# Performance work log

Measured on AMD Instinct MI355X. Metric: run time of the kernel, lower is better.

Reference implementation:

```python
import jax, jax.numpy as jnp
import numpy as np

B, S, D, H = 2, 2048, 768, 12
HD = D // H  # head dim = 64

def setup_inputs() -> dict:
    key = jax.random.key(0)
    ks = jax.random.split(key, 9)
    s = 1.0 / np.sqrt(D)
    return {
        "x": jax.random.normal(ks[0], (B, S, D), dtype=jnp.float32),
        "Wq": jax.random.uniform(ks[1], (D, D), jnp.float32, -s, s),
        "bq": jax.random.uniform(ks[2], (D,), jnp.float32, -s, s),
        "Wk": jax.random.uniform(ks[3], (D, D), jnp.float32, -s, s),
        "bk": jax.random.uniform(ks[4], (D,), jnp.float32, -s, s),
        "Wv": jax.random.uniform(ks[5], (D, D), jnp.float32, -s, s),
        "bv": jax.random.uniform(ks[6], (D,), jnp.float32, -s, s),
        "Wo": jax.random.uniform(ks[7], (D, D), jnp.float32, -s, s),
        "bo": jax.random.uniform(ks[8], (D,), jnp.float32, -s, s),
    }

def reference(x, Wq, bq, Wk, bk, Wv, bv, Wo, bo):
    b, s, _ = x.shape
    # linear projections, split into heads: [b, h, s, hd]
    def proj(W, bias):
        y = x @ W + bias
        return y.reshape(b, s, H, HD).transpose(0, 2, 1, 3)
    q = proj(Wq, bq)
    k = proj(Wk, bk)
    v = proj(Wv, bv)
    scale = 1.0 / np.sqrt(HD).astype(np.float32)
    scores = jnp.einsum('bhqd,bhkd->bhqk', q, k) * scale
    attn = jax.nn.softmax(scores, axis=-1)
    out = jnp.einsum('bhqk,bhkd->bhqd', attn, v)
    out = out.transpose(0, 2, 1, 3).reshape(b, s, D)
    return out @ Wo + bo
```

## Files before the change

kernel.cpp:

```cpp
#include <hip/hip_runtime.h>
#include <math.h>

#define NH 12
#define SEQ 2048
#define DM 768
#define HD 64
#define NB 2
#define MT (NB * SEQ)
#define QSCL 0.18033688011112042591999058512524f

typedef short bf16x8 __attribute__((ext_vector_type(8)));
typedef float f32x16 __attribute__((ext_vector_type(16)));
typedef unsigned u32x2 __attribute__((ext_vector_type(2)));

__device__ __forceinline__ unsigned short bf16_rne(float x) {
    unsigned u = __float_as_uint(x);
    u += 0x7fffu + ((u >> 16) & 1u);
    return (unsigned short)(u >> 16);
}
__device__ __forceinline__ float bf16_tof(short h) {
    return __uint_as_float(((unsigned)(unsigned short)h) << 16);
}
__device__ __forceinline__ unsigned cvtpk(float lo, float hi) {
    unsigned r;
    asm("v_cvt_pk_bf16_f32 %0, %1, %2" : "=v"(r) : "v"(lo), "v"(hi));
    return r;
}

__device__ __forceinline__ void gl_lds16(const void* g, void* s) {
    __builtin_amdgcn_global_load_lds(
        (const __attribute__((address_space(1))) unsigned int*)g,
        (__attribute__((address_space(3))) unsigned int*)s, 16, 0, 0);
}

__device__ __forceinline__ f32x16 mfma32(bf16x8 a, bf16x8 b, f32x16 c) {
    return __builtin_amdgcn_mfma_f32_32x32x16_bf16(a, b, c, 0, 0, 0);
}

__device__ __forceinline__ bf16x8 gfrag(const char* base, int row, int physblk) {
    return *(const bf16x8*)(base + row * 64 + physblk * 16);
}
__device__ __forceinline__ bf16x8 afrag(const short* base, int row, int blk) {
    return *(const bf16x8*)(base + row * 64 + ((blk ^ (row & 7)) << 3));
}

__global__ __launch_bounds__(256)
void conv_all(const float* __restrict__ x,
              const float* __restrict__ Wq, const float* __restrict__ Wk,
              const float* __restrict__ Wv, const float* __restrict__ Wo,
              short* __restrict__ xg, short* __restrict__ wqkv,
              short* __restrict__ wo)
{
    int b = blockIdx.x;
    if (b < 1536) {
        const int idx = b * 256 + threadIdx.x;
        const int m = idx / 96, bk = idx % 96;
        const float* src = x + (size_t)m * DM + bk * 8;
        float4 v0 = *(const float4*)src;
        float4 v1 = *(const float4*)(src + 4);
        const float vv[8] = {v0.x, v0.y, v0.z, v0.w, v1.x, v1.y, v1.z, v1.w};
        union { short s[8]; int4 q; } hh;
#pragma unroll
        for (int j = 0; j < 8; j++) hh.s[j] = (short)bf16_rne(vv[j]);
        const int pb = (bk & ~3) | ((bk & 3) ^ ((m >> 1) & 3));
        *(int4*)(xg + (size_t)m * DM + pb * 8) = hh.q;
    } else {
        b -= 1536;
        const int z = b / 288;
        const float* __restrict__ W = (z == 0) ? Wq : (z == 1) ? Wk : (z == 2) ? Wv : Wo;
        short* __restrict__ wdst = (z == 3) ? wo : (wqkv + (size_t)z * 589824);
        const int idx = (b % 288) * 256 + threadIdx.x;
        const int n = idx % 768, bk = idx / 768;
        union { short s[8]; int4 q; } hh;
#pragma unroll
        for (int j = 0; j < 8; j++) hh.s[j] = (short)bf16_rne(W[(size_t)(bk * 8 + j) * DM + n]);
        const int pb = (bk & ~3) | ((bk & 3) ^ ((n >> 1) & 3));
        *(int4*)(wdst + (size_t)n * DM + pb * 8) = hh.q;
    }
}

template<bool SWAP>
__device__ __forceinline__ void qkv_loop(const char* pA, const char* pB,
                                         char* As, char* Bs,
                                         int t, f32x16* acc)
{
    const int w = t >> 6, l = t & 63;
    const int q32 = l & 31, half = l >> 5;
    const int sel = (q32 >> 1) & 3;
    const int arow  = 32 * (w & 1) + q32;
    const int brow0 = 64 * (w >> 1) + q32;
    char* dA = As + t * 16;
    char* dB = Bs + t * 16;

    uint4 a0, b00, b10;
    uint4 a1, b01, b11;

    a0  = *(const uint4*)(pA);
    b00 = *(const uint4*)(pB);
    b10 = *(const uint4*)(pB + 64 * 1536);
    a1  = *(const uint4*)(pA + 64);
    b01 = *(const uint4*)(pB + 64);
    b11 = *(const uint4*)(pB + 64 * 1536 + 64);
    *(uint4*)dA = a0;
    *(uint4*)dB = b00;
    *(uint4*)(dB + 4096) = b10;
    __syncthreads();

    auto compute = [&](const char* sA, const char* sB) {
#pragma unroll
        for (int s = 0; s < 2; s++) {
            const int blk = (s * 2 + half) ^ sel;
            bf16x8 a  = gfrag(sA, arow, blk);
            bf16x8 b0 = gfrag(sB, brow0, blk);
            bf16x8 b1 = gfrag(sB, brow0 + 32, blk);
            if (SWAP) {
                acc[0] = mfma32(b0, a, acc[0]);
                acc[1] = mfma32(b1, a, acc[1]);
            } else {
                acc[0] = mfma32(a, b0, acc[0]);
                acc[1] = mfma32(a, b1, acc[1]);
            }
        }
    };

    for (int kb = 0; kb < 12; kb++) {
        if (kb < 11) {
            const size_t cb = (size_t)(2 * kb + 2) * 64;
            a0  = *(const uint4*)(pA + cb);
            b00 = *(const uint4*)(pB + cb);
            b10 = *(const uint4*)(pB + 64 * 1536 + cb);
        }
        *(uint4*)(dA + 4096) = a1;
        *(uint4*)(dB + 8192) = b01;
        *(uint4*)(dB + 8192 + 4096) = b11;
        compute(As, Bs);
        __syncthreads();

        if (kb < 11) {
            const size_t cb = (size_t)(2 * kb + 3) * 64;
            a1  = *(const uint4*)(pA + cb);
            b01 = *(const uint4*)(pB + cb);
            b11 = *(const uint4*)(pB + 64 * 1536 + cb);
        }
        if (kb < 11) {
            *(uint4*)dA = a0;
            *(uint4*)dB = b00;
            *(uint4*)(dB + 4096) = b10;
        }
        compute(As + 4096, Bs + 8192);
        __syncthreads();
    }
}

__global__ __launch_bounds__(256)
void gemm_qkv(const short* __restrict__ xg, const short* __restrict__ wqkv,
              const float* __restrict__ bq, const float* __restrict__ bkv,
              const float* __restrict__ bv,
              short* __restrict__ qg, short* __restrict__ kg, short* __restrict__ vg)
{
    const int z = blockIdx.z;
    const short* __restrict__ Bw = wqkv + (size_t)z * 589824;
    const float* __restrict__ bias = (z == 0) ? bq : (z == 1) ? bkv : bv;

    __shared__ char As[8192], Bs[16384];
    const int t = threadIdx.x, w = t >> 6, l = t & 63;
    const int m0 = blockIdx.y * 64, n0 = blockIdx.x * 128;
    const int q32 = l & 31, half = l >> 5;

    const char* pA = (const char*)xg + (size_t)(m0 + (t >> 2)) * 1536 + (t & 3) * 16;
    const char* pB = (const char*)Bw + (size_t)(n0 + (t >> 2)) * 1536 + (t & 3) * 16;

    f32x16 acc[2];
#pragma unroll
    for (int i = 0; i < 2; i++)
#pragma unroll
        for (int r = 0; r < 16; r++) acc[i][r] = 0.f;

    if (z == 2) {
        qkv_loop<false>(pA, pB, As, Bs, t, acc);
        const int nbase = n0 + 64 * (w >> 1);
        const int h = nbase >> 6;
        const int mbase = m0 + 32 * (w & 1) + 4 * half;
        const int bb = mbase >> 11;
#pragma unroll
        for (int nt = 0; nt < 2; nt++) {
            const int hd = 32 * nt + q32;
            const float bia = bias[nbase + hd];
            short* vrow = vg + ((size_t)(bb * NH + h) * HD + hd) * SEQ;
#pragma unroll
            for (int g = 0; g < 4; g++) {
                const int ss0 = (mbase & 2047) + 8 * g;
                union { unsigned short u[4]; uint2 q; } pk;
#pragma unroll
                for (int j = 0; j < 4; j++)
                    pk.u[j] = bf16_rne(acc[nt][4 * g + j] + bia);
                const int blk = ss0 >> 3;
                const int phys = (blk & ~7) | ((blk & 7) ^ (hd & 7));
                *(uint2*)(vrow + phys * 8 + (ss0 & 7)) = pk.q;
            }
        }
    } else {
        qkv_loop<true>(pA, pB, As, Bs, t, acc);
        short* dst = (z == 0) ? qg : kg;
        const float scl = (z == 0) ? QSCL : 1.0f;
        const int mcol = m0 + 32 * (w & 1) + q32;
        const int bb = mcol >> 11, ss = mcol & 2047;
        const int h = (n0 + 64 * (w >> 1)) >> 6;
        short* drow = dst + ((size_t)(bb * NH + h) * SEQ + ss) * HD;
#pragma unroll
        for (int nt = 0; nt < 2; nt++)
#pragma unroll
            for (int g = 0; g < 4; g++) {
                const int hd0 = 32 * nt + 8 * g + 4 * half;
                float4 b4 = *(const float4*)&bias[(h << 6) + hd0];
                const float bb4[4] = {b4.x, b4.y, b4.z, b4.w};
                union { unsigned short u[4]; uint2 q; } pk;
#pragma unroll
                for (int j = 0; j < 4; j++)
                    pk.u[j] = bf16_rne((acc[nt][4 * g + j] + bb4[j]) * scl);
                const int phys = (hd0 >> 3) ^ (ss & 7);
                *(uint2*)(drow + phys * 8 + (hd0 & 7)) = pk.q;
            }
    }
}

__global__ __launch_bounds__(256)
void attn_mfma(const short* __restrict__ qg, const short* __restrict__ kg,
               const short* __restrict__ vg,
               short* __restrict__ opart, float* __restrict__ lpart)
{
    __shared__ short Qs[8192];
    __shared__ short Ks[4096];
    __shared__ short Vt[4096];

    const int t = threadIdx.x, w = t >> 6, l = t & 63;
    const int bh = blockIdx.y, q0 = blockIdx.x * 128, ks = blockIdx.z;
    const char* qp = (const char*)(qg + (size_t)bh * SEQ * HD);
    const char* kp = (const char*)(kg + (size_t)bh * SEQ * HD);
    const char* vp = (const char*)(vg + (size_t)bh * HD * SEQ);
    const int kbase = ks * 512;

#pragma unroll
    for (int i = 0; i < 4; i++)
        gl_lds16(qp + (size_t)(q0 + w * 32 + i * 8) * 128 + l * 16,
                 (char*)Qs + (w * 32 + i * 8) * 128);
#pragma unroll
    for (int i = 0; i < 2; i++) {
        gl_lds16(kp + (size_t)(kbase + w * 16 + i * 8) * 128 + l * 16,
                 (char*)Ks + (w * 16 + i * 8) * 128);
        gl_lds16(vp + (size_t)(w * 16 + i * 8 + (l >> 3)) * 4096 + kbase * 2 + (l & 7) * 16,
                 (char*)Vt + (w * 16 + i * 8) * 128);
    }
    __syncthreads();

    const int half = l >> 5;
    const int q = l & 31;
    bf16x8 qf[4];
#pragma unroll
    for (int s = 0; s < 4; s++)
        qf[s] = afrag(Qs, w * 32 + q, half + s * 2);
    __syncthreads();

    f32x16 oacc[2], lacc;
#pragma unroll
    for (int nt = 0; nt < 2; nt++)
#pragma unroll
        for (int r = 0; r < 16; r++) oacc[nt][r] = 0.f;
#pragma unroll
    for (int r = 0; r < 16; r++) lacc[r] = 0.f;

    bf16x8 onesf;
#pragma unroll
    for (int j = 0; j < 8; j++) onesf[j] = (short)0x3F80;

    for (int kti = 0; kti < 8; kti++) {
        const int cur = kti & 1;
        if (kti < 7) {
            const int kb0 = kbase + (kti + 1) * 64;
            char* kd = cur ? (char*)Ks : (char*)Qs;
            char* vd = cur ? (char*)Vt : (char*)(Qs + 4096);
#pragma unroll
            for (int i = 0; i < 2; i++) {
                gl_lds16(kp + (size_t)(kb0 + w * 16 + i * 8) * 128 + l * 16,
                         kd + (w * 16 + i * 8) * 128);
                gl_lds16(vp + (size_t)(w * 16 + i * 8 + (l >> 3)) * 4096 + kb0 * 2 + (l & 7) * 16,
                         vd + (w * 16 + i * 8) * 128);
            }
        }
        const short* kc = cur ? Qs : Ks;
        const short* vc = cur ? Qs + 4096 : Vt;

        f32x16 sacc[2];
#pragma unroll
        for (int nt = 0; nt < 2; nt++)
#pragma unroll
            for (int r = 0; r < 16; r++) sacc[nt][r] = 0.f;
#pragma unroll
        for (int s = 0; s < 4; s++)
#pragma unroll
            for (int nt = 0; nt < 2; nt++) {
                bf16x8 kf = afrag(kc, nt * 32 + q, half + s * 2);
                sacc[nt] = mfma32(kf, qf[s], sacc[nt]);
            }

#pragma unroll
        for (int nt = 0; nt < 2; nt++)
#pragma unroll
            for (int r = 0; r < 16; r++) sacc[nt][r] = exp2f(sacc[nt][r]);

#pragma unroll
        for (int s = 0; s < 4; s++) {
            const int nt = s >> 1;
            const int rb = (s & 1) * 8;
            const unsigned p0 = cvtpk(sacc[nt][rb + 0], sacc[nt][rb + 1]);
            const unsigned p1 = cvtpk(sacc[nt][rb + 2], sacc[nt][rb + 3]);
            const unsigned p2 = cvtpk(sacc[nt][rb + 4], sacc[nt][rb + 5]);
            const unsigned p3 = cvtpk(sacc[nt][rb + 6], sacc[nt][rb + 7]);
            const u32x2 w02 = __builtin_amdgcn_permlane32_swap(p0, p2, false, false);
            const u32x2 w13 = __builtin_amdgcn_permlane32_swap(p1, p3, false, false);
            union { unsigned u[4]; bf16x8 v; } pf;
            pf.u[0] = w02[0];
            pf.u[1] = w13[0];
            pf.u[2] = w02[1];
            pf.u[3] = w13[1];
            lacc = mfma32(pf.v, onesf, lacc);
#pragma unroll
            for (int nt2 = 0; nt2 < 2; nt2++) {
                bf16x8 vf = afrag(vc, nt2 * 32 + q, half + s * 2);
                oacc[nt2] = mfma32(pf.v, vf, oacc[nt2]);
            }
        }
        __syncthreads();
    }

    const size_t base = (size_t)(ks * 24 + bh) * SEQ;
#pragma unroll
    for (int r = 0; r < 16; r++) {
        const int row = q0 + w * 32 + (r & 3) + 8 * (r >> 2) + 4 * half;
#pragma unroll
        for (int nt = 0; nt < 2; nt++)
            opart[(base + row) * 64 + nt * 32 + q] = (short)bf16_rne(oacc[nt][r]);
        if (q == 0) lpart[base + row] = lacc[r];
    }
}

__global__ __launch_bounds__(256)
void attn_reduce(const short* __restrict__ opart, const float* __restrict__ lpart,
                 short* __restrict__ ag)
{
    const int idx = blockIdx.x * 256 + threadIdx.x;
    const int cg = idx & 7, row = idx >> 3;
    const int bh = row >> 11, s = row & 2047;
    union { short s[8]; int4 q; } a0, a1, a2, a3, o;
    a0.q = *(const int4*)(opart + (((size_t)(0 * 24 + bh) * SEQ) + s) * 64 + cg * 8);
    a1.q = *(const int4*)(opart + (((size_t)(1 * 24 + bh) * SEQ) + s) * 64 + cg * 8);
    a2.q = *(const int4*)(opart + (((size_t)(2 * 24 + bh) * SEQ) + s) * 64 + cg * 8);
    a3.q = *(const int4*)(opart + (((size_t)(3 * 24 + bh) * SEQ) + s) * 64 + cg * 8);
    const float l = lpart[(size_t)(0 * 24 + bh) * SEQ + s]
                  + lpart[(size_t)(1 * 24 + bh) * SEQ + s]
                  + lpart[(size_t)(2 * 24 + bh) * SEQ + s]
                  + lpart[(size_t)(3 * 24 + bh) * SEQ + s];
    const float inv = 1.0f / l;
#pragma unroll
    for (int j = 0; j < 8; j++)
        o.s[j] = (short)bf16_rne((bf16_tof(a0.s[j]) + bf16_tof(a1.s[j])
                                + bf16_tof(a2.s[j]) + bf16_tof(a3.s[j])) * inv);
    const int bb = bh / NH, h = bh % NH;
    const int m = bb * SEQ + s;
    const int blk = h * 8 + cg;
    const int phys = (blk & ~3) | ((blk & 3) ^ ((m >> 1) & 3));
    *(int4*)(ag + (size_t)m * DM + phys * 8) = o.q;
}

__global__ __launch_bounds__(256)
void gemm_out(const short* __restrict__ ag, const short* __restrict__ wt3,
              const float* __restrict__ bias, float* __restrict__ out)
{
    __shared__ char As[8192], Bs[8192];
    const int t = threadIdx.x, w = t >> 6, l = t & 63;
    const int m0 = blockIdx.y * 64, n0 = blockIdx.x * 64;
    const int q32 = l & 31, half = l >> 5;
    const int sel = (q32 >> 1) & 3;

    const char* pA = (const char*)ag  + (size_t)(m0 + (t >> 2)) * 1536 + (t & 3) * 16;
    const char* pB = (const char*)wt3 + (size_t)(n0 + (t >> 2)) * 1536 + (t & 3) * 16;
    char* dA = As + t * 16;
    char* dB = Bs + t * 16;

    const int arow = 32 * (w & 1) + q32;
    const int brow = 32 * (w >> 1) + q32;

    f32x16 acc;
#pragma unroll
    for (int r = 0; r < 16; r++) acc[r] = 0.f;

    uint4 a0, b0, a1, b1;
    a0 = *(const uint4*)(pA);
    b0 = *(const uint4*)(pB);
    a1 = *(const uint4*)(pA + 64);
    b1 = *(const uint4*)(pB + 64);
    *(uint4*)dA = a0;
    *(uint4*)dB = b0;
    __syncthreads();

    for (int kb = 0; kb < 12; kb++) {
        if (kb < 11) {
            const size_t cb = (size_t)(2 * kb + 2) * 64;
            a0 = *(const uint4*)(pA + cb);
            b0 = *(const uint4*)(pB + cb);
        }
        *(uint4*)(dA + 4096) = a1;
        *(uint4*)(dB + 4096) = b1;
#pragma unroll
        for (int s = 0; s < 2; s++) {
            const int blk = (s * 2 + half) ^ sel;
            acc = mfma32(gfrag(Bs, brow, blk), gfrag(As, arow, blk), acc);
        }
        __syncthreads();

        if (kb < 11) {
            const size_t cb = (size_t)(2 * kb + 3) * 64;
            a1 = *(const uint4*)(pA + cb);
            b1 = *(const uint4*)(pB + cb);
        }
        if (kb < 11) {
            *(uint4*)dA = a0;
            *(uint4*)dB = b0;
        }
#pragma unroll
        for (int s = 0; s < 2; s++) {
            const int blk = (s * 2 + half) ^ sel;
            acc = mfma32(gfrag(Bs + 4096, brow, blk), gfrag(As + 4096, arow, blk), acc);
        }
        __syncthreads();
    }

    const int mcol = m0 + 32 * (w & 1) + q32;
    const int nb0 = n0 + 32 * (w >> 1) + 4 * half;
#pragma unroll
    for (int g = 0; g < 4; g++) {
        const int ng = nb0 + 8 * g;
        float4 b4 = *(const float4*)&bias[ng];
        float4 o;
        o.x = acc[4 * g + 0] + b4.x;
        o.y = acc[4 * g + 1] + b4.y;
        o.z = acc[4 * g + 2] + b4.z;
        o.w = acc[4 * g + 3] + b4.w;
        *(float4*)&out[(size_t)mcol * DM + ng] = o;
    }
}

extern "C" void kernel_launch(void* const* d_in, const int* in_sizes, int n_in,
                              void* d_out, int out_size, void* d_ws, size_t ws_size,
                              hipStream_t stream)
{
    const float* x  = (const float*)d_in[0];
    const float* Wq = (const float*)d_in[1];
    const float* bq = (const float*)d_in[2];
    const float* Wk = (const float*)d_in[3];
    const float* bk = (const float*)d_in[4];
    const float* Wv = (const float*)d_in[5];
    const float* bv = (const float*)d_in[6];
    const float* Wo = (const float*)d_in[7];
    const float* bo = (const float*)d_in[8];
    float* out = (float*)d_out;

    const size_t BUF = (size_t)MT * DM;
    short* base  = (short*)d_ws;
    short* wo    = base;
    short* qg    = base + 589824;
    short* kg    = qg + BUF;
    short* vg    = kg + BUF;
    short* opart = vg + BUF;
    float* lpart = (float*)(opart + (size_t)4 * 24 * SEQ * HD);
    short* xg    = opart;
    short* wqkv  = xg + BUF;
    short* ag    = qg;

    conv_all<<<2688, 256, 0, stream>>>(x, Wq, Wk, Wv, Wo, xg, wqkv, wo);
    gemm_qkv<<<dim3(6, 64, 3), 256, 0, stream>>>(xg, wqkv, bq, bk, bv, qg, kg, vg);
    attn_mfma<<<dim3(16, 24, 4), 256, 0, stream>>>(qg, kg, vg, opart, lpart);
    attn_reduce<<<1536, 256, 0, stream>>>(opart, lpart, ag);
    gemm_out<<<dim3(12, 64), 256, 0, stream>>>(ag, wo, bo, out);
}
```

Baseline: 195.1 us.

## Use direct global-to-LDS loads in GEMMs and halve attention key splits

Both GEMM kernels now stage tiles straight from global memory into shared memory with gl_lds16 async loads, double-buffered over 24 k-steps. This replaces register-staged loads followed by LDS stores, saving VGPRs and store instructions. The attention kernel splits keys into 2 chunks of 1024 instead of 4 of 512, so the partial-output buffer and the reduce kernel's reads shrink. The cost is half as many attention blocks (768), which lowers parallelism, and each block runs a longer serial loop.

New measurement: 190.7 us. -2.3%, faster.

```diff
diff --git a/kernel.cpp b/kernel.cpp
--- a/kernel.cpp
+++ b/kernel.cpp
@@ -89,24 +89,24 @@
     const int sel = (q32 >> 1) & 3;
     const int arow  = 32 * (w & 1) + q32;
     const int brow0 = 64 * (w >> 1) + q32;
-    char* dA = As + t * 16;
-    char* dB = Bs + t * 16;
-
-    uint4 a0, b00, b10;
-    uint4 a1, b01, b11;
-
-    a0  = *(const uint4*)(pA);
-    b00 = *(const uint4*)(pB);
-    b10 = *(const uint4*)(pB + 64 * 1536);
-    a1  = *(const uint4*)(pA + 64);
-    b01 = *(const uint4*)(pB + 64);
-    b11 = *(const uint4*)(pB + 64 * 1536 + 64);
-    *(uint4*)dA = a0;
-    *(uint4*)dB = b00;
-    *(uint4*)(dB + 4096) = b10;
+    char* const dA = As + w * 1024;
+    char* const dB = Bs + w * 1024;
+
+    auto stage = [&](int ki, int buf) {
+        const size_t cb = (size_t)ki * 64;
+        gl_lds16(pA + cb, dA + buf * 4096);
+        gl_lds16(pB + cb, dB + buf * 8192);
+        gl_lds16(pB + 64 * 1536 + cb, dB + buf * 8192 + 4096);
+    };
+
+    stage(0, 0);
     __syncthreads();
 
-    auto compute = [&](const char* sA, const char* sB) {
+    for (int ki = 0; ki < 24; ki++) {
+        const int cur = ki & 1;
+        if (ki < 23) stage(ki + 1, cur ^ 1);
+        const char* sA = As + cur * 4096;
+        const char* sB = Bs + cur * 8192;
 #pragma unroll
         for (int s = 0; s < 2; s++) {
             const int blk = (s * 2 + half) ^ sel;
@@ -121,33 +121,6 @@
                 acc[1] = mfma32(a, b1, acc[1]);
             }
         }
-    };
-
-    for (int kb = 0; kb < 12; kb++) {
-        if (kb < 11) {
-            const size_t cb = (size_t)(2 * kb + 2) * 64;
-            a0  = *(const uint4*)(pA + cb);
-            b00 = *(const uint4*)(pB + cb);
-            b10 = *(const uint4*)(pB + 64 * 1536 + cb);
-        }
-        *(uint4*)(dA + 4096) = a1;
-        *(uint4*)(dB + 8192) = b01;
-        *(uint4*)(dB + 8192 + 4096) = b11;
-        compute(As, Bs);
-        __syncthreads();
-
-        if (kb < 11) {
-            const size_t cb = (size_t)(2 * kb + 3) * 64;
-            a1  = *(const uint4*)(pA + cb);
-            b01 = *(const uint4*)(pB + cb);
-            b11 = *(const uint4*)(pB + 64 * 1536 + cb);
-        }
-        if (kb < 11) {
-            *(uint4*)dA = a0;
-            *(uint4*)dB = b00;
-            *(uint4*)(dB + 4096) = b10;
-        }
-        compute(As + 4096, Bs + 8192);
         __syncthreads();
     }
 }
@@ -238,7 +211,7 @@
     const char* qp = (const char*)(qg + (size_t)bh * SEQ * HD);
     const char* kp = (const char*)(kg + (size_t)bh * SEQ * HD);
     const char* vp = (const char*)(vg + (size_t)bh * HD * SEQ);
-    const int kbase = ks * 512;
+    const int kbase = ks * 1024;
 
 #pragma unroll
     for (int i = 0; i < 4; i++)
@@ -273,9 +246,9 @@
 #pragma unroll
     for (int j = 0; j < 8; j++) onesf[j] = (short)0x3F80;
 
-    for (int kti = 0; kti < 8; kti++) {
+    for (int kti = 0; kti < 16; kti++) {
         const int cur = kti & 1;
-        if (kti < 7) {
+        if (kti < 15) {
             const int kb0 = kbase + (kti + 1) * 64;
             char* kd = cur ? (char*)Ks : (char*)Qs;
             char* vd = cur ? (char*)Vt : (char*)(Qs + 4096);
@@ -351,20 +324,13 @@
     const int idx = blockIdx.x * 256 + threadIdx.x;
     const int cg = idx & 7, row = idx >> 3;
     const int bh = row >> 11, s = row & 2047;
-    union { short s[8]; int4 q; } a0, a1, a2, a3, o;
-    a0.q = *(const int4*)(opart + (((size_t)(0 * 24 + bh) * SEQ) + s) * 64 + cg * 8);
-    a1.q = *(const int4*)(opart + (((size_t)(1 * 24 + bh) * SEQ) + s) * 64 + cg * 8);
-    a2.q = *(const int4*)(opart + (((size_t)(2 * 24 + bh) * SEQ) + s) * 64 + cg * 8);
-    a3.q = *(const int4*)(opart + (((size_t)(3 * 24 + bh) * SEQ) + s) * 64 + cg * 8);
-    const float l = lpart[(size_t)(0 * 24 + bh) * SEQ + s]
-                  + lpart[(size_t)(1 * 24 + bh) * SEQ + s]
-                  + lpart[(size_t)(2 * 24 + bh) * SEQ + s]
-                  + lpart[(size_t)(3 * 24 + bh) * SEQ + s];
-    const float inv = 1.0f / l;
+    union { short s[8]; int4 q; } a, b, o;
+    a.q = *(const int4*)(opart + ((size_t)bh * SEQ + s) * 64 + cg * 8);
+    b.q = *(const int4*)(opart + ((size_t)(24 + bh) * SEQ + s) * 64 + cg * 8);
+    const float inv = 1.0f / (lpart[(size_t)bh * SEQ + s] + lpart[(size_t)(24 + bh) * SEQ + s]);
 #pragma unroll
     for (int j = 0; j < 8; j++)
-        o.s[j] = (short)bf16_rne((bf16_tof(a0.s[j]) + bf16_tof(a1.s[j])
-                                + bf16_tof(a2.s[j]) + bf16_tof(a3.s[j])) * inv);
+        o.s[j] = (short)bf16_rne((bf16_tof(a.s[j]) + bf16_tof(b.s[j])) * inv);
     const int bb = bh / NH, h = bh % NH;
     const int m = bb * SEQ + s;
     const int blk = h * 8 + cg;
@@ -384,8 +350,8 @@
 
     const char* pA = (const char*)ag  + (size_t)(m0 + (t >> 2)) * 1536 + (t & 3) * 16;
     const char* pB = (const char*)wt3 + (size_t)(n0 + (t >> 2)) * 1536 + (t & 3) * 16;
-    char* dA = As + t * 16;
-    char* dB = Bs + t * 16;
+    char* const dA = As + w * 1024;
+    char* const dB = Bs + w * 1024;
 
     const int arow = 32 * (w & 1) + q32;
     const int brow = 32 * (w >> 1) + q32;
@@ -394,43 +360,24 @@
 #pragma unroll
     for (int r = 0; r < 16; r++) acc[r] = 0.f;
 
-    uint4 a0, b0, a1, b1;
-    a0 = *(const uint4*)(pA);
-    b0 = *(const uint4*)(pB);
-    a1 = *(const uint4*)(pA + 64);
-    b1 = *(const uint4*)(pB + 64);
-    *(uint4*)dA = a0;
-    *(uint4*)dB = b0;
+    auto stage = [&](int ki, int buf) {
+        const size_t cb = (size_t)ki * 64;
+        gl_lds16(pA + cb, dA + buf * 4096);
+        gl_lds16(pB + cb, dB + buf * 4096);
+    };
+
+    stage(0, 0);
     __syncthreads();
 
-    for (int kb = 0; kb < 12; kb++) {
-        if (kb < 11) {
-            const size_t cb = (size_t)(2 * kb + 2) * 64;
-            a0 = *(const uint4*)(pA + cb);
-            b0 = *(const uint4*)(pB + cb);
-        }
-        *(uint4*)(dA + 4096) = a1;
-        *(uint4*)(dB + 4096) = b1;
+    for (int ki = 0; ki < 24; ki++) {
+        const int cur = ki & 1;
+        if (ki < 23) stage(ki + 1, cur ^ 1);
+        const char* sA = As + cur * 4096;
+        const char* sB = Bs + cur * 4096;
 #pragma unroll
         for (int s = 0; s < 2; s++) {
             const int blk = (s * 2 + half) ^ sel;
-            acc = mfma32(gfrag(Bs, brow, blk), gfrag(As, arow, blk), acc);
-        }
-        __syncthreads();
-
-        if (kb < 11) {
-            const size_t cb = (size_t)(2 * kb + 3) * 64;
-            a1 = *(const uint4*)(pA + cb);
-            b1 = *(const uint4*)(pB + cb);
-        }
-        if (kb < 11) {
-            *(uint4*)dA = a0;
-            *(uint4*)dB = b0;
-        }
-#pragma unroll
-        for (int s = 0; s < 2; s++) {
-            const int blk = (s * 2 + half) ^ sel;
-            acc = mfma32(gfrag(Bs + 4096, brow, blk), gfrag(As + 4096, arow, blk), acc);
+            acc = mfma32(gfrag(sB, brow, blk), gfrag(sA, arow, blk), acc);
         }
         __syncthreads();
     }
@@ -472,14 +419,14 @@
     short* kg    = qg + BUF;
     short* vg    = kg + BUF;
     short* opart = vg + BUF;
-    float* lpart = (float*)(opart + (size_t)4 * 24 * SEQ * HD);
+    float* lpart = (float*)(opart + (size_t)2 * 24 * SEQ * HD);
     short* xg    = opart;
     short* wqkv  = xg + BUF;
     short* ag    = qg;
 
     conv_all<<<2688, 256, 0, stream>>>(x, Wq, Wk, Wv, Wo, xg, wqkv, wo);
     gemm_qkv<<<dim3(6, 64, 3), 256, 0, stream>>>(xg, wqkv, bq, bk, bv, qg, kg, vg);
-    attn_mfma<<<dim3(16, 24, 4), 256, 0, stream>>>(qg, kg, vg, opart, lpart);
+    attn_mfma<<<dim3(16, 24, 2), 256, 0, stream>>>(qg, kg, vg, opart, lpart);
     attn_reduce<<<1536, 256, 0, stream>>>(opart, lpart, ag);
     gemm_out<<<dim3(12, 64), 256, 0, stream>>>(ag, wo, bo, out);
 }
```
